# Optimization experiments

Measured on AMD Instinct MI355X. Metric: run time of the kernel, lower is better.

Reference implementation:

```python
import jax, jax.numpy as jnp
import numpy as np

EPS = 1e-5
ALPHA = 0.7
N_HEADS = 20
N_KV_HEADS = 5
HEAD_DIM = 128


def bitlinear(x, w):
    # absmean ternary quantization per output row: w_t = sign(w)*(|w| > alpha*absmean)
    absw = jnp.abs(w)
    absmean = jnp.mean(absw, axis=1, keepdims=True)            # [out, 1]
    tern = jnp.sign(w) * (absw > ALPHA * absmean).astype(w.dtype)
    # (X @ pos^T - X @ neg^T) * scale == (X @ tern^T) * scale
    return jnp.einsum('...i,oi->...o', x, tern) * absmean[:, 0]


def rmsnorm(x, g):
    var = jnp.mean(jnp.square(x), axis=-1, keepdims=True)
    return x * jax.lax.rsqrt(var + EPS) * g


def rotate_half(x):
    x1, x2 = jnp.split(x, 2, axis=-1)
    return jnp.concatenate([-x2, x1], axis=-1)


def setup_inputs() -> dict:
    key = jax.random.key(0)
    ks = jax.random.split(key, 12)
    h, inter = 2560, 6912
    b, s = 1, 2048
    wscale = 1.0 / np.sqrt(h)
    return {
        'x': jax.random.normal(ks[0], (b, s, h), jnp.float32),
        'cos': jax.random.uniform(ks[1], (1, 1, s, HEAD_DIM), jnp.float32),
        'sin': jax.random.uniform(ks[2], (1, 1, s, HEAD_DIM), jnp.float32),
        'q_w': jax.random.normal(ks[3], (h, h), jnp.float32) * wscale,
        'k_w': jax.random.normal(ks[4], (N_KV_HEADS * HEAD_DIM, h), jnp.float32) * wscale,
        'v_w': jax.random.normal(ks[5], (N_KV_HEADS * HEAD_DIM, h), jnp.float32) * wscale,
        'o_w': jax.random.normal(ks[6], (h, h), jnp.float32) * wscale,
        'gate_w': jax.random.normal(ks[7], (inter, h), jnp.float32) * wscale,
        'up_w': jax.random.normal(ks[8], (inter, h), jnp.float32) * wscale,
        'down_w': jax.random.normal(ks[9], (h, inter), jnp.float32) / np.sqrt(inter),
        'ln1_w': jnp.ones((h,), jnp.float32),
        'ln2_w': jnp.ones((h,), jnp.float32),
    }


def reference(x, cos, sin, q_w, k_w, v_w, o_w, gate_w, up_w, down_w, ln1_w, ln2_w):
    b, s, hdim = x.shape
    residual = x
    h = rmsnorm(x, ln1_w)

    q = bitlinear(h, q_w).reshape(b, s, N_HEADS, HEAD_DIM).transpose(0, 2, 1, 3)
    k = bitlinear(h, k_w).reshape(b, s, N_KV_HEADS, HEAD_DIM).transpose(0, 2, 1, 3)
    v = bitlinear(h, v_w).reshape(b, s, N_KV_HEADS, HEAD_DIM).transpose(0, 2, 1, 3)

    # RoPE
    q = q * cos + rotate_half(q) * sin
    k = k * cos + rotate_half(k) * sin

    # GQA: repeat_interleave kv heads
    n_rep = N_HEADS // N_KV_HEADS
    k = jnp.repeat(k, n_rep, axis=1)
    v = jnp.repeat(v, n_rep, axis=1)

    scale = 1.0 / np.sqrt(HEAD_DIM)
    attn = jnp.einsum('bhqd,bhkd->bhqk', q, k) * scale
    attn = jax.nn.softmax(attn, axis=-1)
    o = jnp.einsum('bhqk,bhkd->bhqd', attn, v)
    o = o.transpose(0, 2, 1, 3).reshape(b, s, hdim)

    x = residual + bitlinear(o, o_w)

    residual = x
    h = rmsnorm(x, ln2_w)
    gate = jnp.square(jax.nn.relu(bitlinear(h, gate_w)))  # relu^2
    x = residual + bitlinear(gate * bitlinear(h, up_w), down_w)
    return x
```

## Files before the change

### kernel.cpp

```cpp
#include <hip/hip_runtime.h>
#include <hip/hip_bf16.h>

typedef unsigned short u16;
typedef short bf16x8 __attribute__((ext_vector_type(8)));
typedef float f32x4 __attribute__((ext_vector_type(4)));

__device__ __forceinline__ u16 f2b(float f) {
    union { __hip_bfloat16 h; u16 u; } cv;
    cv.h = __float2bfloat16(f);
    return cv.u;
}
__device__ __forceinline__ float b2f(u16 u) {
    union { u16 u; __hip_bfloat16 h; } cv;
    cv.u = u;
    return __bfloat162float(cv.h);
}

__device__ __forceinline__ void g2l16(const void* g, void* l) {
    __builtin_amdgcn_global_load_lds(
        (const __attribute__((address_space(1))) unsigned int*)g,
        (__attribute__((address_space(3))) unsigned int*)l, 16, 0, 0);
}

template <int EPT>
__global__ __launch_bounds__(256) void quant_kernel(const float* __restrict__ W,
                                                    u16* __restrict__ T,
                                                    float* __restrict__ scales, int K) {
    const int row = blockIdx.x, tid = threadIdx.x;
    const float* wr = W + (size_t)row * K;
    float v[EPT];
    float s = 0.f;
#pragma unroll
    for (int i = 0; i < EPT; ++i) { v[i] = wr[tid + i * 256]; s += fabsf(v[i]); }
#pragma unroll
    for (int d = 1; d < 64; d <<= 1) s += __shfl_xor(s, d);
    __shared__ float red[4];
    if ((tid & 63) == 0) red[tid >> 6] = s;
    __syncthreads();
    const float absmean = (red[0] + red[1] + red[2] + red[3]) / (float)K;
    const float thr = 0.7f * absmean;
    u16* tr = T + (size_t)row * K;
#pragma unroll
    for (int i = 0; i < EPT; ++i) {
        float w = v[i];
        float t = (fabsf(w) > thr) ? ((w > 0.f) ? 1.f : -1.f) : 0.f;
        tr[tid + i * 256] = f2b(t);
    }
    if (tid == 0) scales[row] = absmean;
}

__global__ __launch_bounds__(256) void rmsnorm_kernel(const float* __restrict__ x,
                                                      const float* __restrict__ g,
                                                      u16* __restrict__ o) {
    const int row = blockIdx.x, tid = threadIdx.x;
    const float* xr = x + (size_t)row * 2560;
    float v[10];
    float s = 0.f;
#pragma unroll
    for (int i = 0; i < 10; ++i) { v[i] = xr[tid + i * 256]; s += v[i] * v[i]; }
#pragma unroll
    for (int d = 1; d < 64; d <<= 1) s += __shfl_xor(s, d);
    __shared__ float red[4];
    if ((tid & 63) == 0) red[tid >> 6] = s;
    __syncthreads();
    const float total = red[0] + red[1] + red[2] + red[3];
    const float rs = rsqrtf(total * (1.f / 2560.f) + 1e-5f);
    u16* orow = o + (size_t)row * 2560;
#pragma unroll
    for (int i = 0; i < 10; ++i) orow[tid + i * 256] = f2b(v[i] * rs * g[tid + i * 256]);
}

template <int MODE>
__global__ __launch_bounds__(512, 4) void gemm_bt(const u16* __restrict__ A,
                                                  const u16* __restrict__ B,
                                                  const float* __restrict__ scale,
                                                  const float* __restrict__ res,
                                                  void* __restrict__ outp,
                                                  int M, int N, int K) {
    __shared__ __align__(16) u16 sA[128 * 64];
    __shared__ __align__(16) u16 sB[128 * 64];
    const int tid = threadIdx.x;
    const int wave = tid >> 6, lane = tid & 63;
    const int lane15 = lane & 15, quad = lane >> 4;
    const int m0 = blockIdx.x * 128, n0 = blockIdx.y * 128;
    const int wm = wave >> 2, wn = wave & 3;

    f32x4 acc[4][2] = {};

    const int r0 = wave * 8 + (lane >> 3);
    const int gcc = (lane & 7) ^ (lane >> 3);
    const size_t aoff = (size_t)(m0 + r0) * K + gcc * 8;
    const size_t boff = (size_t)(n0 + r0) * K + gcc * 8;
    char* ldsA = (char*)sA + wave * 1024;
    char* ldsB = (char*)sB + wave * 1024;
    const int sw = lane15 & 7;

    for (int kt = 0; kt < K; kt += 64) {
        g2l16(A + aoff + kt, ldsA);
        g2l16(A + aoff + (size_t)64 * K + kt, ldsA + 8192);
        g2l16(B + boff + kt, ldsB);
        g2l16(B + boff + (size_t)64 * K + kt, ldsB + 8192);
        __syncthreads();
#pragma unroll
        for (int kc = 0; kc < 2; ++kc) {
            const int pc = ((kc * 4 + quad) ^ sw) * 8;
            bf16x8 af[4], bfr[2];
#pragma unroll
            for (int f = 0; f < 4; ++f)
                af[f] = *(const bf16x8*)&sA[(wm * 64 + f * 16 + lane15) * 64 + pc];
#pragma unroll
            for (int f = 0; f < 2; ++f)
                bfr[f] = *(const bf16x8*)&sB[(wn * 32 + f * 16 + lane15) * 64 + pc];
#pragma unroll
            for (int i = 0; i < 4; ++i)
#pragma unroll
                for (int j = 0; j < 2; ++j)
                    acc[i][j] = __builtin_amdgcn_mfma_f32_16x16x32_bf16(af[i], bfr[j], acc[i][j], 0, 0, 0);
        }
        __syncthreads();
    }

#pragma unroll
    for (int j = 0; j < 2; ++j) {
        const int c = n0 + wn * 32 + j * 16 + lane15;
        const float sc = scale[c];
#pragma unroll
        for (int i = 0; i < 4; ++i) {
            const int rbase = m0 + wm * 64 + i * 16 + quad * 4;
#pragma unroll
            for (int r = 0; r < 4; ++r) {
                const float vv = acc[i][j][r] * sc;
                const size_t idx = (size_t)(rbase + r) * N + c;
                if (MODE == 0) ((u16*)outp)[idx] = f2b(vv);
                else           ((float*)outp)[idx] = res[idx] + vv;
            }
        }
    }
}

__global__ __launch_bounds__(256) void rope_kernel(u16* __restrict__ buf, int stride,
                                                   const float* __restrict__ cs,
                                                   const float* __restrict__ sn, int nh) {
    const int idx = blockIdx.x * 256 + threadIdx.x;
    const int d = idx & 63;
    const int h = (idx >> 6) % nh;
    const int s = idx / (64 * nh);
    const size_t base = (size_t)s * stride + h * 128;
    const float a = b2f(buf[base + d]), b = b2f(buf[base + d + 64]);
    const float c1 = cs[s * 128 + d], s1 = sn[s * 128 + d];
    const float c2 = cs[s * 128 + d + 64], s2 = sn[s * 128 + d + 64];
    buf[base + d] = f2b(a * c1 - b * s1);
    buf[base + d + 64] = f2b(b * c2 + a * s2);
}

__global__ __launch_bounds__(256) void transpose_v_kernel(const u16* __restrict__ V, int stride,
                                                          u16* __restrict__ VT) {
    __shared__ u16 t[128 * 66];
    const int tid = threadIdx.x;
    const int h = blockIdx.y, s0 = blockIdx.x * 64;
#pragma unroll
    for (int i = 0; i < 32; ++i) {
        const int idx = tid + i * 256;
        const int r = idx >> 7, c = idx & 127;
        t[c * 66 + r] = V[(size_t)(s0 + r) * stride + h * 128 + c];
    }
    __syncthreads();
#pragma unroll
    for (int i = 0; i < 32; ++i) {
        const int idx = tid + i * 256;
        const int d = idx >> 6, s = idx & 63;
        VT[((size_t)h * 128 + d) * 2048 + s0 + s] = t[d * 66 + s];
    }
}

__global__ __launch_bounds__(256, 2) void flash_kernel(const u16* __restrict__ Q, int qs,
                                                       const u16* __restrict__ Kb,
                                                       const u16* __restrict__ VT,
                                                       u16* __restrict__ O) {
    __shared__ __align__(16) u16 sQ[64 * 128];
    __shared__ __align__(16) u16 sK[2][64 * 128];
    __shared__ __align__(16) u16 sV[2][128 * 64];
    const int tid = threadIdx.x, wave = tid >> 6, lane = tid & 63;
    const int lane15 = lane & 15, quad = lane >> 4;
    const int head = blockIdx.y, q0 = blockIdx.x * 64, kvh = head >> 2;
    const int sw = lane15 & 7;

    const int rk = wave * 4 + (lane >> 4);
    const int gk = (lane & 15) ^ (rk & 7);
    const u16* kbase = Kb + (size_t)rk * qs + kvh * 128 + gk * 8;
    const int rv = wave * 8 + (lane >> 3);
    const int gv = (lane & 7) ^ (rv & 7);
    const u16* vbase = VT + ((size_t)kvh * 128 + rv) * 2048 + gv * 8;

    auto stage = [&](int k0, int b) {
        char* dK = (char*)(&sK[b][0]) + wave * 1024;
        char* dV = (char*)(&sV[b][0]) + wave * 1024;
#pragma unroll
        for (int s = 0; s < 4; ++s) {
            g2l16(kbase + ((size_t)k0 + s * 16) * qs, dK + s * 4096);
            g2l16(vbase + (size_t)s * 32 * 2048 + k0, dV + s * 4096);
        }
    };

    {
        const int rq = wave * 4 + (lane >> 4);
        const int gq = (lane & 15) ^ (rq & 7);
        const u16* src = Q + (size_t)(q0 + rq) * qs + head * 128 + gq * 8;
        char* dst = (char*)sQ + wave * 1024;
#pragma unroll
        for (int s = 0; s < 4; ++s)
            g2l16(src + (size_t)s * 16 * qs, dst + s * 4096);
        stage(0, 0);
    }
    __syncthreads();
    bf16x8 qf[4];
#pragma unroll
    for (int kc = 0; kc < 4; ++kc)
        qf[kc] = *(const bf16x8*)&sQ[(wave * 16 + lane15) * 128 + ((kc * 4 + quad) ^ sw) * 8];

    float m_i[4], lp[4];
    f32x4 o_acc[8] = {};
#pragma unroll
    for (int r = 0; r < 4; ++r) { m_i[r] = -1e30f; lp[r] = 0.f; }

    const float sl2e = 0.088388347648318447f * 1.4426950408889634f;
    u16* sP = sQ;

    for (int t = 0; t < 32; ++t) {
        const int buf = t & 1;
        if (t < 31) stage((t + 1) * 64, buf ^ 1);
        const u16* sKb = &sK[buf][0];
        const u16* sVb = &sV[buf][0];

        f32x4 sacc[4] = {};
#pragma unroll
        for (int nf = 0; nf < 4; ++nf)
#pragma unroll
            for (int kc = 0; kc < 4; ++kc) {
                const bf16x8 kf = *(const bf16x8*)&sKb[(nf * 16 + lane15) * 128 + ((kc * 4 + quad) ^ sw) * 8];
                sacc[nf] = __builtin_amdgcn_mfma_f32_16x16x32_bf16(qf[kc], kf, sacc[nf], 0, 0, 0);
            }

        float mx[4];
#pragma unroll
        for (int r = 0; r < 4; ++r) {
            float v0 = sacc[0][r] * sl2e, v1 = sacc[1][r] * sl2e;
            float v2 = sacc[2][r] * sl2e, v3 = sacc[3][r] * sl2e;
            sacc[0][r] = v0; sacc[1][r] = v1; sacc[2][r] = v2; sacc[3][r] = v3;
            float m0 = fmaxf(fmaxf(v0, v1), fmaxf(v2, v3));
#pragma unroll
            for (int d = 1; d < 16; d <<= 1) m0 = fmaxf(m0, __shfl_xor(m0, d));
            mx[r] = m0;
        }
        const int upd = (mx[0] > m_i[0]) | (mx[1] > m_i[1]) | (mx[2] > m_i[2]) | (mx[3] > m_i[3]);
        if (__any(upd)) {
#pragma unroll
            for (int r = 0; r < 4; ++r) {
                const float mnew = fmaxf(m_i[r], mx[r]);
                const float alpha = exp2f(m_i[r] - mnew);
                m_i[r] = mnew;
                lp[r] *= alpha;
#pragma unroll
                for (int nf = 0; nf < 8; ++nf) o_acc[nf][r] *= alpha;
            }
        }
#pragma unroll
        for (int r = 0; r < 4; ++r) {
            const float m = m_i[r];
            const float p0 = exp2f(sacc[0][r] - m), p1 = exp2f(sacc[1][r] - m);
            const float p2 = exp2f(sacc[2][r] - m), p3 = exp2f(sacc[3][r] - m);
            sacc[0][r] = p0; sacc[1][r] = p1; sacc[2][r] = p2; sacc[3][r] = p3;
            lp[r] += (p0 + p1) + (p2 + p3);
        }

#pragma unroll
        for (int nf = 0; nf < 4; ++nf) {
            const int cc = nf * 2 + (lane15 >> 3);
            const int pcol = ((cc ^ quad) * 8) + (lane15 & 7);
#pragma unroll
            for (int r = 0; r < 4; ++r)
                sP[(wave * 16 + quad * 4 + r) * 72 + pcol] = f2b(sacc[nf][r]);
        }

        bf16x8 pf[2];
#pragma unroll
        for (int kc = 0; kc < 2; ++kc)
            pf[kc] = *(const bf16x8*)&sP[(wave * 16 + lane15) * 72 + ((kc * 4 + quad) ^ ((lane15 >> 2) & 3)) * 8];
#pragma unroll
        for (int nf = 0; nf < 8; ++nf)
#pragma unroll
            for (int kc = 0; kc < 2; ++kc) {
                const bf16x8 vf = *(const bf16x8*)&sVb[(nf * 16 + lane15) * 64 + ((kc * 4 + quad) ^ sw) * 8];
                o_acc[nf] = __builtin_amdgcn_mfma_f32_16x16x32_bf16(pf[kc], vf, o_acc[nf], 0, 0, 0);
            }
        __syncthreads();
    }

#pragma unroll
    for (int r = 0; r < 4; ++r) {
        float lt = lp[r];
#pragma unroll
        for (int d = 1; d < 16; d <<= 1) lt += __shfl_xor(lt, d);
        const float inv = 1.f / lt;
        const int row = q0 + wave * 16 + quad * 4 + r;
        u16* orow = O + (size_t)row * 2560 + head * 128;
#pragma unroll
        for (int nf = 0; nf < 8; ++nf)
            orow[nf * 16 + lane15] = f2b(o_acc[nf][r] * inv);
    }
}

__global__ __launch_bounds__(256) void glu_kernel(u16* __restrict__ g, const u16* __restrict__ u) {
    const size_t i = ((size_t)blockIdx.x * 256 + threadIdx.x) * 8;
    bf16x8 gv = *(const bf16x8*)(g + i);
    bf16x8 uv = *(const bf16x8*)(u + i);
    bf16x8 ov;
#pragma unroll
    for (int j = 0; j < 8; ++j) {
        float x = b2f((u16)gv[j]);
        x = fmaxf(x, 0.f);
        ov[j] = (short)f2b(x * x * b2f((u16)uv[j]));
    }
    *(bf16x8*)(g + i) = ov;
}

extern "C" void kernel_launch(void* const* d_in, const int* in_sizes, int n_in,
                              void* d_out, int out_size, void* d_ws, size_t ws_size,
                              hipStream_t stream) {
    (void)in_sizes; (void)n_in; (void)out_size; (void)ws_size;
    const float* x      = (const float*)d_in[0];
    const float* cosb   = (const float*)d_in[1];
    const float* sinb   = (const float*)d_in[2];
    const float* q_w    = (const float*)d_in[3];
    const float* k_w    = (const float*)d_in[4];
    const float* v_w    = (const float*)d_in[5];
    const float* o_w    = (const float*)d_in[6];
    const float* gate_w = (const float*)d_in[7];
    const float* up_w   = (const float*)d_in[8];
    const float* down_w = (const float*)d_in[9];
    const float* ln1    = (const float*)d_in[10];
    const float* ln2    = (const float*)d_in[11];

    char* w = (char*)d_ws;
    size_t off = 0;
    auto nxt = [&](size_t sz) { char* p = w + off; off += sz; return p; };
    u16*   TQ = (u16*)nxt(13107200);
    u16*   TK = (u16*)nxt(3276800);
    u16*   TV = (u16*)nxt(3276800);
    u16*   TO = (u16*)nxt(13107200);
    u16*   TB = (u16*)nxt(35389440);
    float* SC = (float*)nxt(91136);
    u16*   H  = (u16*)nxt(10485760);
    u16*   QKV = (u16*)nxt(15728640);
    u16*   VT = (u16*)nxt(2621440);
    float* XM = (float*)nxt(20971520);
    u16*   G  = (u16*)nxt(28311552);
    u16*   U  = TQ;

    quant_kernel<10><<<2560, 256, 0, stream>>>(q_w, TQ, SC + 0, 2560);
    quant_kernel<10><<<640, 256, 0, stream>>>(k_w, TK, SC + 2560, 2560);
    quant_kernel<10><<<640, 256, 0, stream>>>(v_w, TV, SC + 3200, 2560);
    quant_kernel<10><<<2560, 256, 0, stream>>>(o_w, TO, SC + 3840, 2560);
    rmsnorm_kernel<<<2048, 256, 0, stream>>>(x, ln1, H);
    gemm_bt<0><<<dim3(16, 30), 512, 0, stream>>>(H, TQ, SC + 0, nullptr, QKV, 2048, 3840, 2560);
    rope_kernel<<<10240, 256, 0, stream>>>(QKV, 3840, cosb, sinb, 20);
    rope_kernel<<<2560, 256, 0, stream>>>(QKV + 2560, 3840, cosb, sinb, 5);
    transpose_v_kernel<<<dim3(32, 5), 256, 0, stream>>>(QKV + 3200, 3840, VT);
    flash_kernel<<<dim3(32, 20), 256, 0, stream>>>(QKV, 3840, QKV + 2560, VT, H);
    gemm_bt<1><<<dim3(16, 20), 512, 0, stream>>>(H, TO, SC + 3840, x, XM, 2048, 2560, 2560);

    rmsnorm_kernel<<<2048, 256, 0, stream>>>(XM, ln2, H);
    quant_kernel<10><<<6912, 256, 0, stream>>>(gate_w, TB, SC + 6400, 2560);
    gemm_bt<0><<<dim3(16, 54), 512, 0, stream>>>(H, TB, SC + 6400, nullptr, G, 2048, 6912, 2560);
    quant_kernel<10><<<6912, 256, 0, stream>>>(up_w, TB, SC + 13312, 2560);
    gemm_bt<0><<<dim3(16, 54), 512, 0, stream>>>(H, TB, SC + 13312, nullptr, U, 2048, 6912, 2560);
    glu_kernel<<<6912, 256, 0, stream>>>(G, U);
    quant_kernel<27><<<2560, 256, 0, stream>>>(down_w, TB, SC + 20224, 6912);
    gemm_bt<1><<<dim3(16, 20), 512, 0, stream>>>(G, TB, SC + 20224, XM, (float*)d_out, 2048, 2560, 6912);
}
```

Measured before the change: 885.7 us.

## Shrink flash KV tile to 32 keys, raise occupancy, add lazy rescale and setprio

```diff
diff --git a/kernel.cpp b/kernel.cpp
--- a/kernel.cpp
+++ b/kernel.cpp
@@ -173,13 +173,13 @@
     }
 }
 
-__global__ __launch_bounds__(256, 2) void flash_kernel(const u16* __restrict__ Q, int qs,
+__global__ __launch_bounds__(256, 3) void flash_kernel(const u16* __restrict__ Q, int qs,
                                                        const u16* __restrict__ Kb,
                                                        const u16* __restrict__ VT,
                                                        u16* __restrict__ O) {
     __shared__ __align__(16) u16 sQ[64 * 128];
-    __shared__ __align__(16) u16 sK[2][64 * 128];
-    __shared__ __align__(16) u16 sV[2][128 * 64];
+    __shared__ __align__(16) u16 sK[2][32 * 128];
+    __shared__ __align__(16) u16 sV[2][128 * 32];
     const int tid = threadIdx.x, wave = tid >> 6, lane = tid & 63;
     const int lane15 = lane & 15, quad = lane >> 4;
     const int head = blockIdx.y, q0 = blockIdx.x * 64, kvh = head >> 2;
@@ -188,17 +188,17 @@
     const int rk = wave * 4 + (lane >> 4);
     const int gk = (lane & 15) ^ (rk & 7);
     const u16* kbase = Kb + (size_t)rk * qs + kvh * 128 + gk * 8;
-    const int rv = wave * 8 + (lane >> 3);
-    const int gv = (lane & 7) ^ (rv & 7);
+    const int rv = wave * 16 + (lane >> 2);
+    const int gv = (lane & 3) ^ ((lane >> 3) & 3);
     const u16* vbase = VT + ((size_t)kvh * 128 + rv) * 2048 + gv * 8;
 
     auto stage = [&](int k0, int b) {
         char* dK = (char*)(&sK[b][0]) + wave * 1024;
         char* dV = (char*)(&sV[b][0]) + wave * 1024;
 #pragma unroll
-        for (int s = 0; s < 4; ++s) {
+        for (int s = 0; s < 2; ++s) {
             g2l16(kbase + ((size_t)k0 + s * 16) * qs, dK + s * 4096);
-            g2l16(vbase + (size_t)s * 32 * 2048 + k0, dV + s * 4096);
+            g2l16(vbase + (size_t)s * 64 * 2048 + k0, dV + s * 4096);
         }
     };
 
@@ -224,35 +224,38 @@
     for (int r = 0; r < 4; ++r) { m_i[r] = -1e30f; lp[r] = 0.f; }
 
     const float sl2e = 0.088388347648318447f * 1.4426950408889634f;
+    const float THR = 8.0f;
     u16* sP = sQ;
 
-    for (int t = 0; t < 32; ++t) {
+    for (int t = 0; t < 64; ++t) {
         const int buf = t & 1;
-        if (t < 31) stage((t + 1) * 64, buf ^ 1);
+        if (t < 63) stage((t + 1) * 32, buf ^ 1);
         const u16* sKb = &sK[buf][0];
         const u16* sVb = &sV[buf][0];
 
-        f32x4 sacc[4] = {};
-#pragma unroll
-        for (int nf = 0; nf < 4; ++nf)
+        f32x4 sacc[2] = {};
+        __builtin_amdgcn_s_setprio(1);
+#pragma unroll
+        for (int nf = 0; nf < 2; ++nf)
 #pragma unroll
             for (int kc = 0; kc < 4; ++kc) {
                 const bf16x8 kf = *(const bf16x8*)&sKb[(nf * 16 + lane15) * 128 + ((kc * 4 + quad) ^ sw) * 8];
                 sacc[nf] = __builtin_amdgcn_mfma_f32_16x16x32_bf16(qf[kc], kf, sacc[nf], 0, 0, 0);
             }
+        __builtin_amdgcn_s_setprio(0);
 
         float mx[4];
 #pragma unroll
         for (int r = 0; r < 4; ++r) {
             float v0 = sacc[0][r] * sl2e, v1 = sacc[1][r] * sl2e;
-            float v2 = sacc[2][r] * sl2e, v3 = sacc[3][r] * sl2e;
-            sacc[0][r] = v0; sacc[1][r] = v1; sacc[2][r] = v2; sacc[3][r] = v3;
-            float m0 = fmaxf(fmaxf(v0, v1), fmaxf(v2, v3));
+            sacc[0][r] = v0; sacc[1][r] = v1;
+            float m0 = fmaxf(v0, v1);
 #pragma unroll
             for (int d = 1; d < 16; d <<= 1) m0 = fmaxf(m0, __shfl_xor(m0, d));
             mx[r] = m0;
         }
-        const int upd = (mx[0] > m_i[0]) | (mx[1] > m_i[1]) | (mx[2] > m_i[2]) | (mx[3] > m_i[3]);
+        const int upd = (mx[0] > m_i[0] + THR) | (mx[1] > m_i[1] + THR) |
+                        (mx[2] > m_i[2] + THR) | (mx[3] > m_i[3] + THR);
         if (__any(upd)) {
 #pragma unroll
             for (int r = 0; r < 4; ++r) {
@@ -268,31 +271,27 @@
         for (int r = 0; r < 4; ++r) {
             const float m = m_i[r];
             const float p0 = exp2f(sacc[0][r] - m), p1 = exp2f(sacc[1][r] - m);
-            const float p2 = exp2f(sacc[2][r] - m), p3 = exp2f(sacc[3][r] - m);
-            sacc[0][r] = p0; sacc[1][r] = p1; sacc[2][r] = p2; sacc[3][r] = p3;
-            lp[r] += (p0 + p1) + (p2 + p3);
-        }
-
-#pragma unroll
-        for (int nf = 0; nf < 4; ++nf) {
-            const int cc = nf * 2 + (lane15 >> 3);
-            const int pcol = ((cc ^ quad) * 8) + (lane15 & 7);
+            sacc[0][r] = p0; sacc[1][r] = p1;
+            lp[r] += p0 + p1;
+        }
+
+#pragma unroll
+        for (int nf = 0; nf < 2; ++nf) {
+            const int pcol = nf * 16 + lane15;
 #pragma unroll
             for (int r = 0; r < 4; ++r)
-                sP[(wave * 16 + quad * 4 + r) * 72 + pcol] = f2b(sacc[nf][r]);
-        }
-
-        bf16x8 pf[2];
-#pragma unroll
-        for (int kc = 0; kc < 2; ++kc)
-            pf[kc] = *(const bf16x8*)&sP[(wave * 16 + lane15) * 72 + ((kc * 4 + quad) ^ ((lane15 >> 2) & 3)) * 8];
-#pragma unroll
-        for (int nf = 0; nf < 8; ++nf)
-#pragma unroll
-            for (int kc = 0; kc < 2; ++kc) {
-                const bf16x8 vf = *(const bf16x8*)&sVb[(nf * 16 + lane15) * 64 + ((kc * 4 + quad) ^ sw) * 8];
-                o_acc[nf] = __builtin_amdgcn_mfma_f32_16x16x32_bf16(pf[kc], vf, o_acc[nf], 0, 0, 0);
-            }
+                sP[(wave * 16 + quad * 4 + r) * 40 + pcol] = f2b(sacc[nf][r]);
+        }
+
+        const bf16x8 pf = *(const bf16x8*)&sP[(wave * 16 + lane15) * 40 + quad * 8];
+        __builtin_amdgcn_s_setprio(1);
+#pragma unroll
+        for (int nf = 0; nf < 8; ++nf) {
+            const bf16x8 vf = *(const bf16x8*)&sVb[(nf * 16 + lane15) * 32 +
+                                                   ((quad ^ ((lane15 >> 1) & 3))) * 8];
+            o_acc[nf] = __builtin_amdgcn_mfma_f32_16x16x32_bf16(pf, vf, o_acc[nf], 0, 0, 0);
+        }
+        __builtin_amdgcn_s_setprio(0);
         __syncthreads();
     }
 
```

New measurement: 875.7 us. About the same (-1.1%).
